# Kernel optimization log

Measured on AMD Instinct MI355X. Metric: run time of the kernel, lower is better.

Reference implementation:

```python
import jax, jax.numpy as jnp
import numpy as np

N_TOKENS = 50257  # vocab size (init kwarg)


def setup_inputs() -> dict:
    key = jax.random.key(0)
    # [batch, seq] int token ids in [0, N_TOKENS)
    inputs = jax.random.randint(key, (1024, 512), 0, N_TOKENS, dtype=jnp.int32)
    return {"inputs": inputs}


def reference(inputs) -> jnp.ndarray:
    # Faithful math: sum_j one_hot(inputs[b, j], N_TOKENS) -> token count histogram,
    # then drop token id 0 (padding). Implemented as a scatter-add instead of
    # materializing the [B, S, V] one-hot tensor.
    B, S = inputs.shape
    rows = jnp.arange(B, dtype=jnp.int32)[:, None]  # [B, 1] broadcast against [B, S]
    counts = jnp.zeros((B, N_TOKENS), dtype=jnp.float32)
    counts = counts.at[rows, inputs].add(jnp.float32(1.0))  # [B, V]
    return counts[:, 1:]  # drop token id 0, matches [:, 1:] in the original
```

## Files before the change

kernel.cpp:

```cpp
#include <hip/hip_runtime.h>
#include <hip/hip_bf16.h>


#define BATCH 1024
#define SEQ 512
#define VOCAB 50257
#define OUT_COLS (VOCAB - 1)
#define CHUNK 4096
#define NBLK_PER_ROW ((OUT_COLS + CHUNK - 1) / CHUNK)
#define BLOCK 256

__global__ __launch_bounds__(BLOCK) void bow_fused_kernel(
    const int* __restrict__ tokens, float* __restrict__ out) {
    __shared__ unsigned int hist[CHUNK];

    const int c0 = blockIdx.x * CHUNK;
    const int b  = blockIdx.y;
    const int t  = threadIdx.x;

    #pragma unroll
    for (int k = 0; k < CHUNK / (BLOCK * 4); ++k) {
        *(uint4*)&hist[t * 4 + k * BLOCK * 4] = make_uint4(0u, 0u, 0u, 0u);
    }
    __syncthreads();

    const int2 tk = ((const int2*)(tokens + b * SEQ))[t];
    unsigned int c;
    c = (unsigned int)(tk.x - 1 - c0);
    if (c < CHUNK) atomicAdd(&hist[c], 1u);
    c = (unsigned int)(tk.y - 1 - c0);
    if (c < CHUNK) atomicAdd(&hist[c], 1u);
    __syncthreads();

    float* orow = out + (size_t)b * OUT_COLS + c0;
    if (c0 + CHUNK <= OUT_COLS) {
        uint4 h[4];
        #pragma unroll
        for (int k = 0; k < 4; ++k)
            h[k] = *(const uint4*)&hist[t * 4 + k * (BLOCK * 4)];
        #pragma unroll
        for (int k = 0; k < 4; ++k) {
            float4 v = make_float4((float)h[k].x, (float)h[k].y,
                                   (float)h[k].z, (float)h[k].w);
            *(float4*)(orow + t * 4 + k * (BLOCK * 4)) = v;
        }
    } else {
        const int ncols = OUT_COLS - c0;
        for (int i = t * 4; i < ncols; i += BLOCK * 4) {
            uint4 h = *(const uint4*)&hist[i];
            float4 v = make_float4((float)h.x, (float)h.y, (float)h.z, (float)h.w);
            *(float4*)(orow + i) = v;
        }
    }
}

extern "C" void kernel_launch(void* const* d_in, const int* in_sizes, int n_in,
                              void* d_out, int out_size, void* d_ws, size_t ws_size,
                              hipStream_t stream) {
    const int* tokens = (const int*)d_in[0];
    float* out = (float*)d_out;

    dim3 grid(NBLK_PER_ROW, BATCH);
    bow_fused_kernel<<<grid, BLOCK, 0, stream>>>(tokens, out);
}
```

Measured before the change: 198.0 us.

## Split into streaming zero-fill kernel plus global-atomic scatter kernel

Replaces the fused per-row-chunk shared-memory histogram kernel with two kernels. The first is a grid-stride float4 zero-fill of the whole output. The second launches one thread per token and does a global float atomicAdd into that token's count, skipping token 0. This removes the 13-fold rereading of tokens, the LDS clearing and the LDS atomics, so the dominant cost becomes a plain streaming write. In exchange it adds a second kernel launch and scattered global atomics, and the output is written twice where tokens land.

```diff
diff --git a/kernel.cpp b/kernel.cpp
--- a/kernel.cpp
+++ b/kernel.cpp
@@ -1,56 +1,32 @@
 #include <hip/hip_runtime.h>
-#include <hip/hip_bf16.h>
 
 
 #define BATCH 1024
 #define SEQ 512
 #define VOCAB 50257
 #define OUT_COLS (VOCAB - 1)
-#define CHUNK 4096
-#define NBLK_PER_ROW ((OUT_COLS + CHUNK - 1) / CHUNK)
+#define OUT_FLOATS ((size_t)BATCH * OUT_COLS)
+#define OUT_F4 (OUT_FLOATS / 4)
+
+#define ZERO_BLOCKS 2048
 #define BLOCK 256
 
-__global__ __launch_bounds__(BLOCK) void bow_fused_kernel(
+__global__ __launch_bounds__(BLOCK) void bow_zero_kernel(float4* __restrict__ out) {
+    size_t i = (size_t)blockIdx.x * BLOCK + threadIdx.x;
+    const size_t stride = (size_t)ZERO_BLOCKS * BLOCK;
+    const float4 z = make_float4(0.0f, 0.0f, 0.0f, 0.0f);
+    for (; i < OUT_F4; i += stride) {
+        out[i] = z;
+    }
+}
+
+__global__ __launch_bounds__(BLOCK) void bow_scatter_kernel(
     const int* __restrict__ tokens, float* __restrict__ out) {
-    __shared__ unsigned int hist[CHUNK];
-
-    const int c0 = blockIdx.x * CHUNK;
-    const int b  = blockIdx.y;
-    const int t  = threadIdx.x;
-
-    #pragma unroll
-    for (int k = 0; k < CHUNK / (BLOCK * 4); ++k) {
-        *(uint4*)&hist[t * 4 + k * BLOCK * 4] = make_uint4(0u, 0u, 0u, 0u);
-    }
-    __syncthreads();
-
-    const int2 tk = ((const int2*)(tokens + b * SEQ))[t];
-    unsigned int c;
-    c = (unsigned int)(tk.x - 1 - c0);
-    if (c < CHUNK) atomicAdd(&hist[c], 1u);
-    c = (unsigned int)(tk.y - 1 - c0);
-    if (c < CHUNK) atomicAdd(&hist[c], 1u);
-    __syncthreads();
-
-    float* orow = out + (size_t)b * OUT_COLS + c0;
-    if (c0 + CHUNK <= OUT_COLS) {
-        uint4 h[4];
-        #pragma unroll
-        for (int k = 0; k < 4; ++k)
-            h[k] = *(const uint4*)&hist[t * 4 + k * (BLOCK * 4)];
-        #pragma unroll
-        for (int k = 0; k < 4; ++k) {
-            float4 v = make_float4((float)h[k].x, (float)h[k].y,
-                                   (float)h[k].z, (float)h[k].w);
-            *(float4*)(orow + t * 4 + k * (BLOCK * 4)) = v;
-        }
-    } else {
-        const int ncols = OUT_COLS - c0;
-        for (int i = t * 4; i < ncols; i += BLOCK * 4) {
-            uint4 h = *(const uint4*)&hist[i];
-            float4 v = make_float4((float)h.x, (float)h.y, (float)h.z, (float)h.w);
-            *(float4*)(orow + i) = v;
-        }
+    const int gid = blockIdx.x * BLOCK + threadIdx.x;
+    const int tok = tokens[gid];
+    if (tok != 0) {
+        const int b = gid >> 9;
+        atomicAdd(out + (size_t)b * OUT_COLS + (tok - 1), 1.0f);
     }
 }
 
@@ -60,6 +36,7 @@
     const int* tokens = (const int*)d_in[0];
     float* out = (float*)d_out;
 
-    dim3 grid(NBLK_PER_ROW, BATCH);
-    bow_fused_kernel<<<grid, BLOCK, 0, stream>>>(tokens, out);
+    bow_zero_kernel<<<dim3(ZERO_BLOCKS), dim3(BLOCK), 0, stream>>>((float4*)out);
+    bow_scatter_kernel<<<dim3((BATCH * SEQ) / BLOCK), dim3(BLOCK), 0, stream>>>(
+        tokens, out);
 }
```

Measured after the change: 225.3 us. +13.8%, slower.

## Loop each block over half a row's vocab chunks, reusing loaded tokens

Applied to the files above, without the earlier changes.

Replaces the 13x1024 grid of one-chunk blocks with 2048 blocks, each handling half of a batch row and looping over 6-7 vocab chunks. Each block loads its token pair once into registers and reuses it for every chunk, so the repeated token reads, block launches and LDS zeroing setup are no longer paid per chunk. The histogram is cleared in place after being read into registers, and raw s_waitcnt plus s_barrier replaces __syncthreads. In exchange each block serializes more chunks with extra barriers per chunk, and there are fewer blocks to hide store latency in what is mostly a store-bound kernel.

```diff
diff --git a/kernel.cpp b/kernel.cpp
--- a/kernel.cpp
+++ b/kernel.cpp
@@ -1,5 +1,4 @@
 #include <hip/hip_runtime.h>
-#include <hip/hip_bf16.h>
 
 
 #define BATCH 1024
@@ -7,49 +6,77 @@
 #define VOCAB 50257
 #define OUT_COLS (VOCAB - 1)
 #define CHUNK 4096
-#define NBLK_PER_ROW ((OUT_COLS + CHUNK - 1) / CHUNK)
+#define NCHUNK 13
 #define BLOCK 256
 
-__global__ __launch_bounds__(BLOCK) void bow_fused_kernel(
+#define LDS_BAR()                                              \
+    do {                                                       \
+        asm volatile("s_waitcnt lgkmcnt(0)" ::: "memory");     \
+        __builtin_amdgcn_s_barrier();                          \
+        asm volatile("" ::: "memory");                         \
+    } while (0)
+
+__global__ __launch_bounds__(BLOCK) void bow_persistent_kernel(
     const int* __restrict__ tokens, float* __restrict__ out) {
     __shared__ unsigned int hist[CHUNK];
 
-    const int c0 = blockIdx.x * CHUNK;
-    const int b  = blockIdx.y;
-    const int t  = threadIdx.x;
+    const int t = threadIdx.x;
+    const int b = blockIdx.x >> 1;
+    const int h = blockIdx.x & 1;
+    const int cbeg = h ? 7 : 0;
+    const int cend = h ? NCHUNK : 7;
 
+    const uint4 z4 = make_uint4(0u, 0u, 0u, 0u);
     #pragma unroll
-    for (int k = 0; k < CHUNK / (BLOCK * 4); ++k) {
-        *(uint4*)&hist[t * 4 + k * BLOCK * 4] = make_uint4(0u, 0u, 0u, 0u);
-    }
-    __syncthreads();
+    for (int k = 0; k < 4; ++k)
+        *(uint4*)&hist[t * 4 + k * (BLOCK * 4)] = z4;
 
-    const int2 tk = ((const int2*)(tokens + b * SEQ))[t];
-    unsigned int c;
-    c = (unsigned int)(tk.x - 1 - c0);
-    if (c < CHUNK) atomicAdd(&hist[c], 1u);
-    c = (unsigned int)(tk.y - 1 - c0);
-    if (c < CHUNK) atomicAdd(&hist[c], 1u);
-    __syncthreads();
+    const int2 tk = ((const int2*)(tokens + (size_t)b * SEQ))[t];
+    const unsigned int cx = (unsigned int)(tk.x - 1);
+    const unsigned int cy = (unsigned int)(tk.y - 1);
 
-    float* orow = out + (size_t)b * OUT_COLS + c0;
-    if (c0 + CHUNK <= OUT_COLS) {
-        uint4 h[4];
+    LDS_BAR();
+
+    for (int c = cbeg; c < cend; ++c) {
+        const unsigned int c0 = (unsigned int)c * CHUNK;
+
+        unsigned int r;
+        r = cx - c0;
+        if (r < CHUNK) atomicAdd(&hist[r], 1u);
+        r = cy - c0;
+        if (r < CHUNK) atomicAdd(&hist[r], 1u);
+
+        LDS_BAR();
+
+        uint4 hreg[4];
         #pragma unroll
         for (int k = 0; k < 4; ++k)
-            h[k] = *(const uint4*)&hist[t * 4 + k * (BLOCK * 4)];
+            hreg[k] = *(const uint4*)&hist[t * 4 + k * (BLOCK * 4)];
         #pragma unroll
-        for (int k = 0; k < 4; ++k) {
-            float4 v = make_float4((float)h[k].x, (float)h[k].y,
-                                   (float)h[k].z, (float)h[k].w);
-            *(float4*)(orow + t * 4 + k * (BLOCK * 4)) = v;
-        }
-    } else {
-        const int ncols = OUT_COLS - c0;
-        for (int i = t * 4; i < ncols; i += BLOCK * 4) {
-            uint4 h = *(const uint4*)&hist[i];
-            float4 v = make_float4((float)h.x, (float)h.y, (float)h.z, (float)h.w);
-            *(float4*)(orow + i) = v;
+        for (int k = 0; k < 4; ++k)
+            *(uint4*)&hist[t * 4 + k * (BLOCK * 4)] = z4;
+
+        LDS_BAR();
+
+        float* orow = out + (size_t)b * OUT_COLS + c0;
+        if (c0 + CHUNK <= (unsigned int)OUT_COLS) {
+            #pragma unroll
+            for (int k = 0; k < 4; ++k) {
+                float4 v = make_float4((float)hreg[k].x, (float)hreg[k].y,
+                                       (float)hreg[k].z, (float)hreg[k].w);
+                *(float4*)(orow + t * 4 + k * (BLOCK * 4)) = v;
+            }
+        } else {
+            const int ncols = OUT_COLS - (int)c0;
+            #pragma unroll
+            for (int k = 0; k < 4; ++k) {
+                const int i = t * 4 + k * (BLOCK * 4);
+                if (i < ncols) {
+                    float4 v = make_float4((float)hreg[k].x, (float)hreg[k].y,
+                                           (float)hreg[k].z, (float)hreg[k].w);
+                    *(float4*)(orow + i) = v;
+                }
+            }
         }
     }
 }
@@ -60,6 +87,5 @@
     const int* tokens = (const int*)d_in[0];
     float* out = (float*)d_out;
 
-    dim3 grid(NBLK_PER_ROW, BATCH);
-    bow_fused_kernel<<<grid, BLOCK, 0, stream>>>(tokens, out);
+    bow_persistent_kernel<<<dim3(BATCH * 2), dim3(BLOCK), 0, stream>>>(tokens, out);
 }
```

Measured after the change: 195.3 us. About the same (-1.4%).
